# Kernel tuning notes

Hardware: AMD Instinct MI355X
Metric: run time of the kernel (lower is better)

## Reference

```python
import jax, jax.numpy as jnp
import numpy as np

SMOOTH = 9.0   # self.labmda
EPS = 1e-8
MASK_VAL = -1.0

I, R, D = 64, 36, 1024   # n_image, n_regions, d
C, W = 64, 32            # n_caption, max_n_word


def setup_inputs() -> dict:
    key = jax.random.key(0)
    k1, k2, k3, k4 = jax.random.split(key, 4)
    imgs = jax.random.normal(k1, (I, R, D), dtype=jnp.float32)
    caps = jax.random.normal(k2, (C, W, D), dtype=jnp.float32)
    img_lens = jax.random.randint(k3, (I,), 1, R + 1)
    cap_lens = jnp.maximum(jax.random.randint(k4, (C,), 0, W + 1), 4)
    return {"imgs": imgs, "caps": caps, "img_lens": img_lens, "cap_lens": cap_lens}


def reference(imgs, caps, img_lens, cap_lens):
    # imgs: (I,R,D) images/regions; caps: (C,W,D); cap_lens: (C,)
    # Vectorized over captions: padded word positions are masked so the
    # per-caption word-dim l2norm matches the ragged torch loop exactly.
    wmask = jnp.arange(W)[None, :] < cap_lens[:, None]          # (C,W)
    wmask_f = wmask.astype(imgs.dtype)

    # attn[c,i,w,r] = <caps[c,w], imgs[i,r]>  (torch: bmm(context, queryT))
    attn = jnp.einsum('ird,cwd->ciwr', imgs, caps)              # (C,I,W,R)
    attn = jax.nn.leaky_relu(attn, 0.1)
    attn = attn * wmask_f[:, None, :, None]                     # zero padded words
    # l2norm over word dim (torch l2norm(attn, 2) on (I,R,W)): eps after sqrt
    norm_w = jnp.sqrt(jnp.sum(attn * attn, axis=2, keepdims=True)) + EPS
    attn = attn / norm_w
    # temperature-scaled softmax over regions
    attn = jax.nn.softmax(attn * SMOOTH, axis=3)                # (C,I,W,R)

    # weighted context per word, l2-normalized over feature dim
    wctx = jnp.einsum('ciwr,ird->ciwd', attn, imgs)             # (C,I,W,D)
    wctx = wctx / (jnp.sqrt(jnp.sum(wctx * wctx, axis=-1, keepdims=True)) + EPS)

    # cosine similarity between the word and its attended context
    cap_e = caps[:, None, :, :]                                 # (C,1,W,D)
    w12 = jnp.sum(cap_e * wctx, axis=-1)                        # (C,I,W)
    w1 = jnp.sqrt(jnp.sum(cap_e * cap_e, axis=-1))
    w2 = jnp.sqrt(jnp.sum(wctx * wctx, axis=-1))
    sim = w12 / jnp.maximum(w1 * w2, EPS)                       # (C,I,W)

    sim = jnp.where(wmask[:, None, :], sim, MASK_VAL)
    return jnp.transpose(sim, (1, 0, 2))                        # (I,C,W)
```

## Files before the change

### kernel.cpp

```cpp
#include <hip/hip_runtime.h>
#include <hip/hip_bf16.h>

#define IDIM 64
#define RDIM 36
#define DDIM 1024
#define CDIM 64
#define WDIM 32
#define SMOOTH 9.0f
#define EPSF 1e-8f

typedef __bf16 bf16_t;
typedef __bf16 bf16x8 __attribute__((ext_vector_type(8)));
typedef __bf16 bf16x4 __attribute__((ext_vector_type(4)));
typedef float f32x4 __attribute__((ext_vector_type(4)));

#define MFMA16(a, b, c) __builtin_amdgcn_mfma_f32_16x16x32_bf16((a), (b), (c), 0, 0, 0)

#define IMGSB_OFF 0
#define IMGSB_BYTES (IDIM * 4 * 8 * 3 * 512 * 2)
#define CAPSA_OFF (IMGSB_OFF + IMGSB_BYTES)
#define CAPSA_BYTES (CDIM * 4 * 8 * 2 * 512 * 2)
#define GF_OFF    (CAPSA_OFF + CAPSA_BYTES)
#define GF_BYTES  (IDIM * 384 * 8 * 2)
#define CAPN_OFF  (GF_OFF + GF_BYTES)

__global__ __launch_bounds__(256) void prep_fused(
    const float* __restrict__ imgs, const float* __restrict__ caps,
    bf16_t* __restrict__ imgsB, bf16_t* __restrict__ capsA,
    bf16_t* __restrict__ Gfrag, float* __restrict__ capnorm) {
  __shared__ __align__(16) char smem0[4 * 48 * 49 * 4];
  __shared__ __align__(16) bf16_t fragL[4][12288];
  bf16_t* ldsb = (bf16_t*)smem0;
  float (*part)[48][49] = (float(*)[48][49])smem0;

  int b = blockIdx.x, tid = threadIdx.x;
  int wv = tid >> 6, ln = tid & 63;
  int l15 = ln & 15, qd = ln >> 4;

  if (b < 64) {
    int i = b;
    for (int wvk = 0; wvk < 4; ++wvk) {
      const float* src = imgs + (size_t)i * RDIM * DDIM + wvk * 256;
#pragma unroll
      for (int rep = 0; rep < 9; ++rep) {
        int idx = rep * 256 + tid;
        int row = idx >> 6, q = idx & 63;
        float4 v = *(const float4*)(src + (size_t)row * DDIM + q * 4);
        bf16x4 p;
        p[0] = (bf16_t)v.x; p[1] = (bf16_t)v.y; p[2] = (bf16_t)v.z; p[3] = (bf16_t)v.w;
        *(bf16x4*)&ldsb[row * 264 + q * 4] = p;
      }
      __syncthreads();
      bf16_t* dst = imgsB + (size_t)(i * 4 + wvk) * 12288;
#pragma unroll
      for (int rep = 0; rep < 6; ++rep) {
        int u = rep * 256 + tid;
        int kk = u / 192, rem = u - kk * 192;
        int nt = rem >> 6, lane = rem & 63, qd2 = lane >> 4, l152 = lane & 15;
        int row = nt * 16 + l152;
        bf16x8 p;
        if (row < 36) {
          p = *(const bf16x8*)&ldsb[row * 264 + kk * 32 + qd2 * 8];
        } else {
#pragma unroll
          for (int j = 0; j < 8; ++j) p[j] = (bf16_t)0.0f;
        }
        *(bf16x8*)(dst + (size_t)u * 8) = p;
        *(bf16x8*)&fragL[wvk][u * 8] = p;
      }
      __syncthreads();
    }
    f32x4 acc[3][3];
#pragma unroll
    for (int mt = 0; mt < 3; ++mt)
#pragma unroll
      for (int nt = 0; nt < 3; ++nt) {
        f32x4 zf = {0.f, 0.f, 0.f, 0.f};
        acc[mt][nt] = zf;
      }
#pragma unroll
    for (int kk = 0; kk < 8; ++kk) {
      bf16x8 a[3];
#pragma unroll
      for (int nt = 0; nt < 3; ++nt)
        a[nt] = *(const bf16x8*)&fragL[wv][((kk * 3 + nt) * 64 + ln) * 8];
#pragma unroll
      for (int mt = 0; mt < 3; ++mt)
#pragma unroll
        for (int nt = 0; nt < 3; ++nt)
          acc[mt][nt] = MFMA16(a[mt], a[nt], acc[mt][nt]);
    }
#pragma unroll
    for (int mt = 0; mt < 3; ++mt)
#pragma unroll
      for (int nt = 0; nt < 3; ++nt)
#pragma unroll
        for (int rg = 0; rg < 4; ++rg)
          part[wv][mt * 16 + qd * 4 + rg][nt * 16 + l15] = acc[mt][nt][rg];
    __syncthreads();
    for (int idx = tid; idx < 384; idx += 256) {
      int kk = idx / 192;
      int rem = idx - kk * 192;
      int nt = rem >> 6, lnn = rem & 63;
      int qd2 = lnn >> 4, l152 = lnn & 15;
      int n = nt * 16 + l152;
      bf16x8 pk;
#pragma unroll
      for (int j = 0; j < 8; ++j) {
        int k = kk * 32 + qd2 * 8 + j;
        float v = (k < 48) ? (part[0][k][n] + part[1][k][n] + part[2][k][n] + part[3][k][n]) : 0.f;
        pk[j] = (bf16_t)v;
      }
      *(bf16x8*)(Gfrag + ((size_t)i * 384 + idx) * 8) = pk;
    }
  } else {
    int c = b - 64;
    const float* src = caps + (size_t)c * WDIM * DDIM;
    float ss[8];
#pragma unroll
    for (int rep = 0; rep < 8; ++rep) ss[rep] = 0.f;
    for (int wvk = 0; wvk < 4; ++wvk) {
#pragma unroll
      for (int rep = 0; rep < 8; ++rep) {
        int idx = rep * 256 + tid;
        int row = idx >> 6, q = idx & 63;
        float4 v = *(const float4*)(src + (size_t)row * DDIM + wvk * 256 + q * 4);
        ss[rep] += v.x * v.x + v.y * v.y + v.z * v.z + v.w * v.w;
        bf16x4 p;
        p[0] = (bf16_t)v.x; p[1] = (bf16_t)v.y; p[2] = (bf16_t)v.z; p[3] = (bf16_t)v.w;
        *(bf16x4*)&ldsb[row * 264 + q * 4] = p;
      }
      __syncthreads();
      bf16_t* dst = capsA + (size_t)(c * 4 + wvk) * 8192;
#pragma unroll
      for (int rep = 0; rep < 4; ++rep) {
        int u = rep * 256 + tid;
        int kk = u >> 7, rem = u & 127;
        int mt = rem >> 6, lane = rem & 63, qd2 = lane >> 4, l152 = lane & 15;
        int row = mt * 16 + l152;
        bf16x8 p = *(const bf16x8*)&ldsb[row * 264 + kk * 32 + qd2 * 8];
        *(bf16x8*)(dst + (size_t)u * 8) = p;
      }
      __syncthreads();
    }
#pragma unroll
    for (int rep = 0; rep < 8; ++rep) {
      float s = ss[rep];
#pragma unroll
      for (int off = 32; off >= 1; off >>= 1) s += __shfl_xor(s, off, 64);
      if (ln == rep) capnorm[c * 32 + rep * 4 + wv] = sqrtf(s);
    }
  }
}

__global__ __launch_bounds__(256, 4) void main_kernel(
    const bf16_t* __restrict__ capsA, const bf16_t* __restrict__ imgsB,
    const bf16_t* __restrict__ Gfrag, const float* __restrict__ capnorm,
    const int* __restrict__ cap_lens, float* __restrict__ out) {
  __shared__ __align__(16) bf16_t ldsB[2][6144];

  int bx = blockIdx.x;
  int wv = threadIdx.x >> 6, ln = threadIdx.x & 63;
  int l15 = ln & 15, qd = ln >> 4;
  int xcd = bx & 7, rest = bx >> 3;
  int ih = rest & 7, cq = rest >> 3;
  int i = xcd * 8 + ih;
  int c = cq * 4 + wv;
  int clen = cap_lens[c];

  const bf16_t* Ab = capsA + (size_t)c * 32768;
  const bf16_t* Bb = imgsB + (size_t)i * 49152;

  bf16x8 t0, t1, t2;
  {
    const bf16_t* gp = Bb + wv * 1536 + ln * 8;
    t0 = *(const bf16x8*)(gp);
    t1 = *(const bf16x8*)(gp + 512);
    t2 = *(const bf16x8*)(gp + 1024);
    bf16_t* lp = &ldsB[0][wv * 1536 + ln * 8];
    *(bf16x8*)(lp) = t0;
    *(bf16x8*)(lp + 512) = t1;
    *(bf16x8*)(lp + 1024) = t2;
  }
  __syncthreads();

  f32x4 acc[2][3];
#pragma unroll
  for (int mt = 0; mt < 2; ++mt)
#pragma unroll
    for (int nt = 0; nt < 3; ++nt) {
      f32x4 zf = {0.f, 0.f, 0.f, 0.f};
      acc[mt][nt] = zf;
    }

  for (int ch = 0; ch < 8; ++ch) {
    int p = ch & 1;
    if (ch < 7) {
      const bf16_t* gp = Bb + (ch + 1) * 6144 + wv * 1536 + ln * 8;
      t0 = *(const bf16x8*)(gp);
      t1 = *(const bf16x8*)(gp + 512);
      t2 = *(const bf16x8*)(gp + 1024);
    }
#pragma unroll
    for (int j = 0; j < 4; ++j) {
      int s = ch * 4 + j;
      const bf16_t* ap = Ab + (size_t)s * 1024 + ln * 8;
      bf16x8 a0 = *(const bf16x8*)(ap);
      bf16x8 a1 = *(const bf16x8*)(ap + 512);
      const bf16_t* lp = &ldsB[p][j * 1536 + ln * 8];
      bf16x8 b0 = *(const bf16x8*)(lp);
      bf16x8 b1 = *(const bf16x8*)(lp + 512);
      bf16x8 b2 = *(const bf16x8*)(lp + 1024);
      acc[0][0] = MFMA16(a0, b0, acc[0][0]);
      acc[0][1] = MFMA16(a0, b1, acc[0][1]);
      acc[0][2] = MFMA16(a0, b2, acc[0][2]);
      acc[1][0] = MFMA16(a1, b0, acc[1][0]);
      acc[1][1] = MFMA16(a1, b1, acc[1][1]);
      acc[1][2] = MFMA16(a1, b2, acc[1][2]);
    }
    if (ch < 7) {
      bf16_t* lp = &ldsB[1 - p][wv * 1536 + ln * 8];
      *(bf16x8*)(lp) = t0;
      *(bf16x8*)(lp + 512) = t1;
      *(bf16x8*)(lp + 1024) = t2;
    }
    __syncthreads();
  }

  const bf16_t* Gb = Gfrag + (size_t)i * 3072;
  bf16x8 ga[2][3];
#pragma unroll
  for (int kk = 0; kk < 2; ++kk)
#pragma unroll
    for (int nt = 0; nt < 3; ++nt)
      ga[kk][nt] = *(const bf16x8*)(Gb + ((size_t)(kk * 3 + nt) * 64 + ln) * 8);

  float sinv[3];
#pragma unroll
  for (int nt = 0; nt < 3; ++nt) {
    bool padn = (nt == 2) && (l15 >= 4);
    float ns = 0.f;
#pragma unroll
    for (int mt = 0; mt < 2; ++mt)
#pragma unroll
      for (int rg = 0; rg < 4; ++rg) {
        float v = acc[mt][nt][rg];
        float l = (v > 0.f) ? v : 0.1f * v;
        int m = mt * 16 + qd * 4 + rg;
        if (m >= clen || padn) l = 0.f;
        ns += l * l;
      }
    ns += __shfl_xor(ns, 16, 64);
    ns += __shfl_xor(ns, 32, 64);
    sinv[nt] = SMOOTH / (sqrtf(ns) + EPSF);
  }

  float Srow[2][4];
#pragma unroll
  for (int mt = 0; mt < 2; ++mt)
#pragma unroll
    for (int rg = 0; rg < 4; ++rg) {
      int m = mt * 16 + qd * 4 + rg;
      bool mrow = (m >= clen);
      float z[3];
#pragma unroll
      for (int nt = 0; nt < 3; ++nt) {
        float v = acc[mt][nt][rg];
        float l = (v > 0.f) ? v : 0.1f * v;
        if (mrow) l = 0.f;
        float zz = l * sinv[nt];
        if (nt == 2 && l15 >= 4) zz = -1e30f;
        z[nt] = zz;
      }
      float mx = fmaxf(fmaxf(z[0], z[1]), z[2]);
#pragma unroll
      for (int off = 1; off < 16; off <<= 1) mx = fmaxf(mx, __shfl_xor(mx, off, 64));
      float e[3], es = 0.f;
#pragma unroll
      for (int nt = 0; nt < 3; ++nt) {
        e[nt] = __expf(z[nt] - mx);
        es += e[nt];
      }
#pragma unroll
      for (int off = 1; off < 16; off <<= 1) es += __shfl_xor(es, off, 64);
      float inv = 1.0f / es;
      float sac = 0.f;
#pragma unroll
      for (int nt = 0; nt < 3; ++nt) {
        float a = e[nt] * inv;
        sac += a * acc[mt][nt][rg];
        acc[mt][nt][rg] = a;
      }
#pragma unroll
      for (int off = 1; off < 16; off <<= 1) sac += __shfl_xor(sac, off, 64);
      Srow[mt][rg] = sac;
    }

  bf16_t* as = &ldsB[0][0] + wv * 2304;
#pragma unroll
  for (int mt = 0; mt < 2; ++mt)
#pragma unroll
    for (int nt = 0; nt < 3; ++nt)
#pragma unroll
      for (int rg = 0; rg < 4; ++rg)
        as[(mt * 16 + qd * 4 + rg) * 72 + nt * 16 + l15] = (bf16_t)acc[mt][nt][rg];
  {
    bf16x8 z8;
#pragma unroll
    for (int q = 0; q < 8; ++q) z8[q] = (bf16_t)0.0f;
    *(bf16x8*)(as + (ln >> 1) * 72 + 48 + (ln & 1) * 8) = z8;
  }
  bf16x8 fa[2][2];
#pragma unroll
  for (int mt = 0; mt < 2; ++mt)
#pragma unroll
    for (int kk = 0; kk < 2; ++kk)
      fa[mt][kk] = *(const bf16x8*)(as + (mt * 16 + l15) * 72 + kk * 32 + qd * 8);

  f32x4 y[2][3];
#pragma unroll
  for (int mt = 0; mt < 2; ++mt)
#pragma unroll
    for (int nt = 0; nt < 3; ++nt) {
      f32x4 zf = {0.f, 0.f, 0.f, 0.f};
      y[mt][nt] = zf;
    }
#pragma unroll
  for (int kk = 0; kk < 2; ++kk)
#pragma unroll
    for (int mt = 0; mt < 2; ++mt)
#pragma unroll
      for (int nt = 0; nt < 3; ++nt)
        y[mt][nt] = MFMA16(fa[mt][kk], ga[kk][nt], y[mt][nt]);

  float n2row[2][4];
#pragma unroll
  for (int mt = 0; mt < 2; ++mt)
#pragma unroll
    for (int rg = 0; rg < 4; ++rg) {
      float nn = 0.f;
#pragma unroll
      for (int nt = 0; nt < 3; ++nt) nn += y[mt][nt][rg] * acc[mt][nt][rg];
#pragma unroll
      for (int off = 1; off < 16; off <<= 1) nn += __shfl_xor(nn, off, 64);
      n2row[mt][rg] = nn;
    }

  if (l15 < 2) {
    int mt = l15;
    f32x4 cn = *(const f32x4*)(capnorm + c * 32 + mt * 16 + qd * 4);
    f32x4 o;
#pragma unroll
    for (int rg = 0; rg < 4; ++rg) {
      float n2v = fmaxf(n2row[mt][rg], 0.f);
      float nrm = sqrtf(n2v);
      float den = nrm + EPSF;
      float w12 = Srow[mt][rg] / den;
      float w2 = nrm / den;
      float sim = w12 / fmaxf(cn[rg] * w2, EPSF);
      int m = mt * 16 + qd * 4 + rg;
      if (m >= clen) sim = -1.0f;
      o[rg] = sim;
    }
    *(f32x4*)(out + ((size_t)i * CDIM + c) * WDIM + mt * 16 + qd * 4) = o;
  }
}

extern "C" void kernel_launch(void* const* d_in, const int* in_sizes, int n_in,
                              void* d_out, int out_size, void* d_ws, size_t ws_size,
                              hipStream_t stream) {
  const float* imgs = (const float*)d_in[0];
  const float* caps = (const float*)d_in[1];
  const int* cap_lens = (const int*)d_in[3];
  float* out = (float*)d_out;

  char* ws = (char*)d_ws;
  bf16_t* imgsB = (bf16_t*)(ws + IMGSB_OFF);
  bf16_t* capsA = (bf16_t*)(ws + CAPSA_OFF);
  bf16_t* Gfrag = (bf16_t*)(ws + GF_OFF);
  float* capnorm = (float*)(ws + CAPN_OFF);

  prep_fused<<<128, 256, 0, stream>>>(imgs, caps, imgsB, capsA, Gfrag, capnorm);
  main_kernel<<<1024, 256, 0, stream>>>(capsA, imgsB, Gfrag, capnorm, cap_lens, out);
}
```

Before: 99.08 us.

## Split prep kernel across D-chunks with atomic Gram and norm accumulation

The prep kernel now launches one block per (image or caption, quarter of D) instead of one block per image or caption, giving 512 blocks in place of 128. Each block handles its own 256-wide slice, so the serial loop over the four chunks is removed. Partial Gram matrices and squared caption norms are combined with float atomicAdd into buffers zeroed by a memset. The main kernel converts the fp32 Gram into bf16 fragments on load and takes a sqrt of the caption norm. This adds a memset launch, atomic traffic, and run-to-run nondeterminism in the summation order.

```diff
diff --git a/kernel.cpp b/kernel.cpp
--- a/kernel.cpp
+++ b/kernel.cpp
@@ -17,19 +17,20 @@
 #define MFMA16(a, b, c) __builtin_amdgcn_mfma_f32_16x16x32_bf16((a), (b), (c), 0, 0, 0)
 
 #define IMGSB_OFF 0
-#define IMGSB_BYTES (IDIM * 4 * 8 * 3 * 512 * 2)
+#define IMGSB_BYTES (IDIM * 4 * 12288 * 2)
 #define CAPSA_OFF (IMGSB_OFF + IMGSB_BYTES)
-#define CAPSA_BYTES (CDIM * 4 * 8 * 2 * 512 * 2)
-#define GF_OFF    (CAPSA_OFF + CAPSA_BYTES)
-#define GF_BYTES  (IDIM * 384 * 8 * 2)
-#define CAPN_OFF  (GF_OFF + GF_BYTES)
-
-__global__ __launch_bounds__(256) void prep_fused(
+#define CAPSA_BYTES (CDIM * 4 * 8192 * 2)
+#define GRAM_OFF (CAPSA_OFF + CAPSA_BYTES)
+#define GRAM_BYTES (IDIM * 48 * 48 * 4)
+#define CAPN2_OFF (GRAM_OFF + GRAM_BYTES)
+#define CAPN2_BYTES (CDIM * WDIM * 4)
+
+__global__ __launch_bounds__(256, 2) void prep2(
     const float* __restrict__ imgs, const float* __restrict__ caps,
     bf16_t* __restrict__ imgsB, bf16_t* __restrict__ capsA,
-    bf16_t* __restrict__ Gfrag, float* __restrict__ capnorm) {
+    float* __restrict__ Gramf, float* __restrict__ capn2) {
   __shared__ __align__(16) char smem0[4 * 48 * 49 * 4];
-  __shared__ __align__(16) bf16_t fragL[4][12288];
+  __shared__ __align__(16) bf16_t fragL[12288];
   bf16_t* ldsb = (bf16_t*)smem0;
   float (*part)[48][49] = (float(*)[48][49])smem0;
 
@@ -37,39 +38,37 @@
   int wv = tid >> 6, ln = tid & 63;
   int l15 = ln & 15, qd = ln >> 4;
 
-  if (b < 64) {
-    int i = b;
-    for (int wvk = 0; wvk < 4; ++wvk) {
-      const float* src = imgs + (size_t)i * RDIM * DDIM + wvk * 256;
-#pragma unroll
-      for (int rep = 0; rep < 9; ++rep) {
-        int idx = rep * 256 + tid;
-        int row = idx >> 6, q = idx & 63;
-        float4 v = *(const float4*)(src + (size_t)row * DDIM + q * 4);
-        bf16x4 p;
-        p[0] = (bf16_t)v.x; p[1] = (bf16_t)v.y; p[2] = (bf16_t)v.z; p[3] = (bf16_t)v.w;
-        *(bf16x4*)&ldsb[row * 264 + q * 4] = p;
-      }
-      __syncthreads();
-      bf16_t* dst = imgsB + (size_t)(i * 4 + wvk) * 12288;
-#pragma unroll
-      for (int rep = 0; rep < 6; ++rep) {
-        int u = rep * 256 + tid;
-        int kk = u / 192, rem = u - kk * 192;
-        int nt = rem >> 6, lane = rem & 63, qd2 = lane >> 4, l152 = lane & 15;
-        int row = nt * 16 + l152;
-        bf16x8 p;
-        if (row < 36) {
-          p = *(const bf16x8*)&ldsb[row * 264 + kk * 32 + qd2 * 8];
-        } else {
-#pragma unroll
-          for (int j = 0; j < 8; ++j) p[j] = (bf16_t)0.0f;
-        }
-        *(bf16x8*)(dst + (size_t)u * 8) = p;
-        *(bf16x8*)&fragL[wvk][u * 8] = p;
-      }
-      __syncthreads();
-    }
+  if (b < 256) {
+    int i = b >> 2, wvk = b & 3;
+    const float* src = imgs + (size_t)i * RDIM * DDIM + wvk * 256;
+#pragma unroll
+    for (int rep = 0; rep < 9; ++rep) {
+      int idx = rep * 256 + tid;
+      int row = idx >> 6, q = idx & 63;
+      float4 v = *(const float4*)(src + (size_t)row * DDIM + q * 4);
+      bf16x4 p;
+      p[0] = (bf16_t)v.x; p[1] = (bf16_t)v.y; p[2] = (bf16_t)v.z; p[3] = (bf16_t)v.w;
+      *(bf16x4*)&ldsb[row * 264 + q * 4] = p;
+    }
+    __syncthreads();
+    bf16_t* dst = imgsB + (size_t)(i * 4 + wvk) * 12288;
+#pragma unroll
+    for (int rep = 0; rep < 6; ++rep) {
+      int u = rep * 256 + tid;
+      int kk = u / 192, rem = u - kk * 192;
+      int nt = rem >> 6, lane = rem & 63, qd2 = lane >> 4, l152 = lane & 15;
+      int row = nt * 16 + l152;
+      bf16x8 p;
+      if (row < 36) {
+        p = *(const bf16x8*)&ldsb[row * 264 + kk * 32 + qd2 * 8];
+      } else {
+#pragma unroll
+        for (int j = 0; j < 8; ++j) p[j] = (bf16_t)0.0f;
+      }
+      *(bf16x8*)(dst + (size_t)u * 8) = p;
+      *(bf16x8*)&fragL[u * 8] = p;
+    }
+    __syncthreads();
     f32x4 acc[3][3];
 #pragma unroll
     for (int mt = 0; mt < 3; ++mt)
@@ -79,11 +78,12 @@
         acc[mt][nt] = zf;
       }
 #pragma unroll
-    for (int kk = 0; kk < 8; ++kk) {
+    for (int t = 0; t < 2; ++t) {
+      int kk = wv * 2 + t;
       bf16x8 a[3];
 #pragma unroll
       for (int nt = 0; nt < 3; ++nt)
-        a[nt] = *(const bf16x8*)&fragL[wv][((kk * 3 + nt) * 64 + ln) * 8];
+        a[nt] = *(const bf16x8*)&fragL[((kk * 3 + nt) * 64 + ln) * 8];
 #pragma unroll
       for (int mt = 0; mt < 3; ++mt)
 #pragma unroll
@@ -98,64 +98,55 @@
         for (int rg = 0; rg < 4; ++rg)
           part[wv][mt * 16 + qd * 4 + rg][nt * 16 + l15] = acc[mt][nt][rg];
     __syncthreads();
-    for (int idx = tid; idx < 384; idx += 256) {
-      int kk = idx / 192;
-      int rem = idx - kk * 192;
-      int nt = rem >> 6, lnn = rem & 63;
-      int qd2 = lnn >> 4, l152 = lnn & 15;
-      int n = nt * 16 + l152;
-      bf16x8 pk;
-#pragma unroll
-      for (int j = 0; j < 8; ++j) {
-        int k = kk * 32 + qd2 * 8 + j;
-        float v = (k < 48) ? (part[0][k][n] + part[1][k][n] + part[2][k][n] + part[3][k][n]) : 0.f;
-        pk[j] = (bf16_t)v;
-      }
-      *(bf16x8*)(Gfrag + ((size_t)i * 384 + idx) * 8) = pk;
+    float* gp = Gramf + (size_t)i * 2304;
+#pragma unroll
+    for (int it = 0; it < 9; ++it) {
+      int u = it * 256 + tid;
+      int r = u / 48, cc = u - r * 48;
+      float v = part[0][r][cc] + part[1][r][cc] + part[2][r][cc] + part[3][r][cc];
+      atomicAdd(gp + u, v);
     }
   } else {
-    int c = b - 64;
-    const float* src = caps + (size_t)c * WDIM * DDIM;
+    int bb = b - 256;
+    int c = bb >> 2, wvk = bb & 3;
+    const float* src = caps + (size_t)c * WDIM * DDIM + wvk * 256;
     float ss[8];
 #pragma unroll
     for (int rep = 0; rep < 8; ++rep) ss[rep] = 0.f;
-    for (int wvk = 0; wvk < 4; ++wvk) {
-#pragma unroll
-      for (int rep = 0; rep < 8; ++rep) {
-        int idx = rep * 256 + tid;
-        int row = idx >> 6, q = idx & 63;
-        float4 v = *(const float4*)(src + (size_t)row * DDIM + wvk * 256 + q * 4);
-        ss[rep] += v.x * v.x + v.y * v.y + v.z * v.z + v.w * v.w;
-        bf16x4 p;
-        p[0] = (bf16_t)v.x; p[1] = (bf16_t)v.y; p[2] = (bf16_t)v.z; p[3] = (bf16_t)v.w;
-        *(bf16x4*)&ldsb[row * 264 + q * 4] = p;
-      }
-      __syncthreads();
-      bf16_t* dst = capsA + (size_t)(c * 4 + wvk) * 8192;
-#pragma unroll
-      for (int rep = 0; rep < 4; ++rep) {
-        int u = rep * 256 + tid;
-        int kk = u >> 7, rem = u & 127;
-        int mt = rem >> 6, lane = rem & 63, qd2 = lane >> 4, l152 = lane & 15;
-        int row = mt * 16 + l152;
-        bf16x8 p = *(const bf16x8*)&ldsb[row * 264 + kk * 32 + qd2 * 8];
-        *(bf16x8*)(dst + (size_t)u * 8) = p;
-      }
-      __syncthreads();
+#pragma unroll
+    for (int rep = 0; rep < 8; ++rep) {
+      int idx = rep * 256 + tid;
+      int row = idx >> 6, q = idx & 63;
+      float4 v = *(const float4*)(src + (size_t)row * DDIM + q * 4);
+      ss[rep] += v.x * v.x + v.y * v.y + v.z * v.z + v.w * v.w;
+      bf16x4 p;
+      p[0] = (bf16_t)v.x; p[1] = (bf16_t)v.y; p[2] = (bf16_t)v.z; p[3] = (bf16_t)v.w;
+      *(bf16x4*)&ldsb[row * 264 + q * 4] = p;
+    }
+    __syncthreads();
+    bf16_t* dst = capsA + (size_t)(c * 4 + wvk) * 8192;
+#pragma unroll
+    for (int rep = 0; rep < 4; ++rep) {
+      int u = rep * 256 + tid;
+      int kk = u >> 7, rem = u & 127;
+      int mt = rem >> 6, lane = rem & 63, qd2 = lane >> 4, l152 = lane & 15;
+      int row = mt * 16 + l152;
+      bf16x8 p = *(const bf16x8*)&ldsb[row * 264 + kk * 32 + qd2 * 8];
+      *(bf16x8*)(dst + (size_t)u * 8) = p;
     }
 #pragma unroll
     for (int rep = 0; rep < 8; ++rep) {
       float s = ss[rep];
 #pragma unroll
       for (int off = 32; off >= 1; off >>= 1) s += __shfl_xor(s, off, 64);
-      if (ln == rep) capnorm[c * 32 + rep * 4 + wv] = sqrtf(s);
+      if (ln == 0) atomicAdd(&capn2[c * 32 + rep * 4 + wv], s);
     }
   }
 }
 
 __global__ __launch_bounds__(256, 4) void main_kernel(
     const bf16_t* __restrict__ capsA, const bf16_t* __restrict__ imgsB,
-    const bf16_t* __restrict__ Gfrag, const float* __restrict__ capnorm,
+    const float* __restrict__ Gramf, const float* __restrict__ capn2,
     const int* __restrict__ cap_lens, float* __restrict__ out) {
   __shared__ __align__(16) bf16_t ldsB[2][6144];
 
@@ -227,13 +218,27 @@
     __syncthreads();
   }
 
-  const bf16_t* Gb = Gfrag + (size_t)i * 3072;
+  const float* Gb = Gramf + (size_t)i * 2304;
   bf16x8 ga[2][3];
 #pragma unroll
   for (int kk = 0; kk < 2; ++kk)
 #pragma unroll
-    for (int nt = 0; nt < 3; ++nt)
-      ga[kk][nt] = *(const bf16x8*)(Gb + ((size_t)(kk * 3 + nt) * 64 + ln) * 8);
+    for (int nt = 0; nt < 3; ++nt) {
+      bf16x8 g;
+      if (kk == 1 && qd >= 2) {
+#pragma unroll
+        for (int j = 0; j < 8; ++j) g[j] = (bf16_t)0.0f;
+      } else {
+        const float* gp = Gb + (nt * 16 + l15) * 48 + kk * 32 + qd * 8;
+        f32x4 u0 = *(const f32x4*)(gp);
+        f32x4 u1 = *(const f32x4*)(gp + 4);
+        g[0] = (bf16_t)u0[0]; g[1] = (bf16_t)u0[1];
+        g[2] = (bf16_t)u0[2]; g[3] = (bf16_t)u0[3];
+        g[4] = (bf16_t)u1[0]; g[5] = (bf16_t)u1[1];
+        g[6] = (bf16_t)u1[2]; g[7] = (bf16_t)u1[3];
+      }
+      ga[kk][nt] = g;
+    }
 
   float sinv[3];
 #pragma unroll
@@ -348,16 +353,17 @@
 
   if (l15 < 2) {
     int mt = l15;
-    f32x4 cn = *(const f32x4*)(capnorm + c * 32 + mt * 16 + qd * 4);
+    f32x4 cn2 = *(const f32x4*)(capn2 + c * 32 + mt * 16 + qd * 4);
     f32x4 o;
 #pragma unroll
     for (int rg = 0; rg < 4; ++rg) {
+      float cnv = sqrtf(cn2[rg]);
       float n2v = fmaxf(n2row[mt][rg], 0.f);
       float nrm = sqrtf(n2v);
       float den = nrm + EPSF;
       float w12 = Srow[mt][rg] / den;
       float w2 = nrm / den;
-      float sim = w12 / fmaxf(cn[rg] * w2, EPSF);
+      float sim = w12 / fmaxf(cnv * w2, EPSF);
       int m = mt * 16 + qd * 4 + rg;
       if (m >= clen) sim = -1.0f;
       o[rg] = sim;
@@ -377,9 +383,10 @@
   char* ws = (char*)d_ws;
   bf16_t* imgsB = (bf16_t*)(ws + IMGSB_OFF);
   bf16_t* capsA = (bf16_t*)(ws + CAPSA_OFF);
-  bf16_t* Gfrag = (bf16_t*)(ws + GF_OFF);
-  float* capnorm = (float*)(ws + CAPN_OFF);
-
-  prep_fused<<<128, 256, 0, stream>>>(imgs, caps, imgsB, capsA, Gfrag, capnorm);
-  main_kernel<<<1024, 256, 0, stream>>>(capsA, imgsB, Gfrag, capnorm, cap_lens, out);
+  float* Gramf = (float*)(ws + GRAM_OFF);
+  float* capn2 = (float*)(ws + CAPN2_OFF);
+
+  hipMemsetAsync(ws + GRAM_OFF, 0, GRAM_BYTES + CAPN2_BYTES, stream);
+  prep2<<<512, 256, 0, stream>>>(imgs, caps, imgsB, capsA, Gramf, capn2);
+  main_kernel<<<1024, 256, 0, stream>>>(capsA, imgsB, Gramf, capn2, cap_lens, out);
 }
```

Measured after the change: 103.3 us. 1.04x slower.
